# Kernel optimization log

Measured on AMD Instinct MI355X. Metric: run time of the kernel, lower is better.

The kernel has to match this reference:

```python
import jax, jax.numpy as jnp
import numpy as np


def setup_inputs() -> dict:
    key = jax.random.key(0)
    ks = jax.random.split(key, 5)
    B, T, D = 2048, 128, 512
    x = jax.random.normal(ks[0], (B, T, D), dtype=jnp.float32)
    h0 = jnp.zeros((1, B, 1), dtype=jnp.float32)
    w_ih = jax.random.normal(ks[1], (3, D), dtype=jnp.float32) * (1.0 / np.sqrt(D))
    w_hh = jax.random.normal(ks[2], (3, 1), dtype=jnp.float32)
    b_ih = jax.random.normal(ks[3], (3,), dtype=jnp.float32) * 0.1
    b_hh = jax.random.normal(ks[4], (3,), dtype=jnp.float32) * 0.1
    return {"x": x, "h0": h0, "w_ih": w_ih, "w_hh": w_hh, "b_ih": b_ih, "b_hh": b_hh}


def reference(x, h0, w_ih, w_hh, b_ih, b_hh):
    # PyTorch GRU, hidden_size=1, num_layers=1, batch_first=True.
    # Precompute the input projection for all timesteps: [B, T, 3] (gates r, z, n).
    gi = jnp.einsum('btd,gd->btg', x, w_ih) + b_ih

    def step(h, gi_t):
        # h: [B, 1]; gi_t: [B, 3]
        gh = h @ w_hh.T + b_hh                      # [B, 3]
        r = jax.nn.sigmoid(gi_t[:, 0:1] + gh[:, 0:1])
        z = jax.nn.sigmoid(gi_t[:, 1:2] + gh[:, 1:2])
        n = jnp.tanh(gi_t[:, 2:3] + r * gh[:, 2:3])
        h_new = (1.0 - z) * n + z * h               # [B, 1]
        return h_new, h_new

    _, outs = jax.lax.scan(step, h0[0], jnp.swapaxes(gi, 0, 1))  # [T, B, 1]
    out = jnp.swapaxes(outs, 0, 1)                                # [B, T, 1]
    # out.mean(0) -> [T, 1]; split into T scalars ('t0'..'tT-1') == squeezed vector [T]
    return out.mean(axis=0).squeeze(-1)
```

## Files before the change

kernel.cpp:

```cpp
#include <hip/hip_runtime.h>
#include <math.h>

#define BB 2048
#define TT 128
#define DD 512
#define NTASK (BB * TT)

__global__ __launch_bounds__(256) void gi_kernel(const float* __restrict__ x,
                                                 const float* __restrict__ w_ih,
                                                 float* __restrict__ gr,
                                                 float* __restrict__ gz,
                                                 float* __restrict__ gn) {
    const int lane   = threadIdx.x & 63;
    const int wave   = blockIdx.x * (blockDim.x >> 6) + (threadIdx.x >> 6);
    const int nwaves = (gridDim.x * blockDim.x) >> 6;

    const int doff = lane * 8;
    const float4 wr0 = *(const float4*)(w_ih + 0 * DD + doff);
    const float4 wr1 = *(const float4*)(w_ih + 0 * DD + doff + 4);
    const float4 wz0 = *(const float4*)(w_ih + 1 * DD + doff);
    const float4 wz1 = *(const float4*)(w_ih + 1 * DD + doff + 4);
    const float4 wn0 = *(const float4*)(w_ih + 2 * DD + doff);
    const float4 wn1 = *(const float4*)(w_ih + 2 * DD + doff + 4);

    for (int task = wave; task < NTASK; task += nwaves) {
        const float* xp = x + (size_t)task * DD + doff;
        const float4 x0 = *(const float4*)(xp);
        const float4 x1 = *(const float4*)(xp + 4);

        float sr = x0.x * wr0.x + x0.y * wr0.y + x0.z * wr0.z + x0.w * wr0.w +
                   x1.x * wr1.x + x1.y * wr1.y + x1.z * wr1.z + x1.w * wr1.w;
        float sz = x0.x * wz0.x + x0.y * wz0.y + x0.z * wz0.z + x0.w * wz0.w +
                   x1.x * wz1.x + x1.y * wz1.y + x1.z * wz1.z + x1.w * wz1.w;
        float sn = x0.x * wn0.x + x0.y * wn0.y + x0.z * wn0.z + x0.w * wn0.w +
                   x1.x * wn1.x + x1.y * wn1.y + x1.z * wn1.z + x1.w * wn1.w;

        #pragma unroll
        for (int off = 32; off > 0; off >>= 1) {
            sr += __shfl_xor(sr, off);
            sz += __shfl_xor(sz, off);
            sn += __shfl_xor(sn, off);
        }

        if (lane == 0) {
            const int b = task >> 7;
            const int t = task & (TT - 1);
            gr[t * BB + b] = sr;
            gz[t * BB + b] = sz;
            gn[t * BB + b] = sn;
        }
    }
}

__global__ __launch_bounds__(64) void gru_kernel(const float* __restrict__ gr,
                                                 const float* __restrict__ gz,
                                                 const float* __restrict__ gn,
                                                 const float* __restrict__ h0,
                                                 const float* __restrict__ w_hh,
                                                 const float* __restrict__ b_ih,
                                                 const float* __restrict__ b_hh,
                                                 float* __restrict__ out) {
    const int b = blockIdx.x * 64 + threadIdx.x;

    const float whr = w_hh[0], whz = w_hh[1], whn = w_hh[2];
    const float br  = b_ih[0] + b_hh[0];
    const float bz  = b_ih[1] + b_hh[1];
    const float bin_= b_ih[2];
    const float bhn = b_hh[2];

    float h = h0[b];

    for (int t = 0; t < TT; ++t) {
        const float ir  = gr[t * BB + b] + br  + h * whr;
        const float iz  = gz[t * BB + b] + bz  + h * whz;
        const float ghn = h * whn + bhn;

        const float r = 1.0f / (1.0f + expf(-ir));
        const float z = 1.0f / (1.0f + expf(-iz));
        const float n = tanhf(gn[t * BB + b] + b_ih[2] - bin_ + bin_ + r * ghn);

        h = (1.0f - z) * n + z * h;

        float s = h;
        #pragma unroll
        for (int off = 32; off > 0; off >>= 1) s += __shfl_xor(s, off);
        if (threadIdx.x == 0) atomicAdd(out + t, s * (1.0f / (float)BB));
    }
}

extern "C" void kernel_launch(void* const* d_in, const int* in_sizes, int n_in,
                              void* d_out, int out_size, void* d_ws, size_t ws_size,
                              hipStream_t stream) {
    const float* x    = (const float*)d_in[0];
    const float* h0   = (const float*)d_in[1];
    const float* w_ih = (const float*)d_in[2];
    const float* w_hh = (const float*)d_in[3];
    const float* b_ih = (const float*)d_in[4];
    const float* b_hh = (const float*)d_in[5];
    float* out = (float*)d_out;

    float* gr = (float*)d_ws;
    float* gz = gr + NTASK;
    float* gn = gz + NTASK;

    hipMemsetAsync(d_out, 0, (size_t)out_size * sizeof(float), stream);

    gi_kernel<<<2048, 256, 0, stream>>>(x, w_ih, gr, gz, gn);
    gru_kernel<<<BB / 64, 64, 0, stream>>>(gr, gz, gn, h0, w_hh, b_ih, b_hh, out);
}
```

Measured before the change: 804.6 us.

## Process two rows per wave in projection, fold output zeroing, block-reduce in GRU

The input-projection kernel now handles two (b,t) rows per wave iteration, putting more loads in flight to better saturate memory bandwidth on the large x read. The memset launch is removed and the output is zeroed inside the first kernel. The recurrent kernel uses 256-thread blocks with a shared-memory reduction, which cuts the number of atomics per timestep but adds two barriers per step and leaves only 8 blocks in flight.

```diff
diff --git a/kernel.cpp b/kernel.cpp
--- a/kernel.cpp
+++ b/kernel.cpp
@@ -10,7 +10,10 @@
                                                  const float* __restrict__ w_ih,
                                                  float* __restrict__ gr,
                                                  float* __restrict__ gz,
-                                                 float* __restrict__ gn) {
+                                                 float* __restrict__ gn,
+                                                 float* __restrict__ out) {
+    if (blockIdx.x == 0 && threadIdx.x < TT) out[threadIdx.x] = 0.0f;
+
     const int lane   = threadIdx.x & 63;
     const int wave   = blockIdx.x * (blockDim.x >> 6) + (threadIdx.x >> 6);
     const int nwaves = (gridDim.x * blockDim.x) >> 6;
@@ -23,10 +26,14 @@
     const float4 wn0 = *(const float4*)(w_ih + 2 * DD + doff);
     const float4 wn1 = *(const float4*)(w_ih + 2 * DD + doff + 4);
 
-    for (int task = wave; task < NTASK; task += nwaves) {
-        const float* xp = x + (size_t)task * DD + doff;
+    for (int task = wave; task < NTASK; task += 2 * nwaves) {
+        const int task2 = task + nwaves;
+        const float* xp  = x + (size_t)task  * DD + doff;
+        const float* xq  = x + (size_t)task2 * DD + doff;
         const float4 x0 = *(const float4*)(xp);
         const float4 x1 = *(const float4*)(xp + 4);
+        const float4 y0 = *(const float4*)(xq);
+        const float4 y1 = *(const float4*)(xq + 4);
 
         float sr = x0.x * wr0.x + x0.y * wr0.y + x0.z * wr0.z + x0.w * wr0.w +
                    x1.x * wr1.x + x1.y * wr1.y + x1.z * wr1.z + x1.w * wr1.w;
@@ -34,57 +41,86 @@
                    x1.x * wz1.x + x1.y * wz1.y + x1.z * wz1.z + x1.w * wz1.w;
         float sn = x0.x * wn0.x + x0.y * wn0.y + x0.z * wn0.z + x0.w * wn0.w +
                    x1.x * wn1.x + x1.y * wn1.y + x1.z * wn1.z + x1.w * wn1.w;
+        float tr = y0.x * wr0.x + y0.y * wr0.y + y0.z * wr0.z + y0.w * wr0.w +
+                   y1.x * wr1.x + y1.y * wr1.y + y1.z * wr1.z + y1.w * wr1.w;
+        float tz = y0.x * wz0.x + y0.y * wz0.y + y0.z * wz0.z + y0.w * wz0.w +
+                   y1.x * wz1.x + y1.y * wz1.y + y1.z * wz1.z + y1.w * wz1.w;
+        float tn = y0.x * wn0.x + y0.y * wn0.y + y0.z * wn0.z + y0.w * wn0.w +
+                   y1.x * wn1.x + y1.y * wn1.y + y1.z * wn1.z + y1.w * wn1.w;
 
         #pragma unroll
         for (int off = 32; off > 0; off >>= 1) {
             sr += __shfl_xor(sr, off);
             sz += __shfl_xor(sz, off);
             sn += __shfl_xor(sn, off);
+            tr += __shfl_xor(tr, off);
+            tz += __shfl_xor(tz, off);
+            tn += __shfl_xor(tn, off);
         }
 
         if (lane == 0) {
-            const int b = task >> 7;
-            const int t = task & (TT - 1);
-            gr[t * BB + b] = sr;
-            gz[t * BB + b] = sz;
-            gn[t * BB + b] = sn;
+            {
+                const int b = task >> 7, t = task & (TT - 1);
+                gr[t * BB + b] = sr;
+                gz[t * BB + b] = sz;
+                gn[t * BB + b] = sn;
+            }
+            {
+                const int b = task2 >> 7, t = task2 & (TT - 1);
+                gr[t * BB + b] = tr;
+                gz[t * BB + b] = tz;
+                gn[t * BB + b] = tn;
+            }
         }
     }
 }
 
-__global__ __launch_bounds__(64) void gru_kernel(const float* __restrict__ gr,
-                                                 const float* __restrict__ gz,
-                                                 const float* __restrict__ gn,
-                                                 const float* __restrict__ h0,
-                                                 const float* __restrict__ w_hh,
-                                                 const float* __restrict__ b_ih,
-                                                 const float* __restrict__ b_hh,
-                                                 float* __restrict__ out) {
-    const int b = blockIdx.x * 64 + threadIdx.x;
+__global__ __launch_bounds__(256) void gru_kernel(const float* __restrict__ gr,
+                                                  const float* __restrict__ gz,
+                                                  const float* __restrict__ gn,
+                                                  const float* __restrict__ h0,
+                                                  const float* __restrict__ w_hh,
+                                                  const float* __restrict__ b_ih,
+                                                  const float* __restrict__ b_hh,
+                                                  float* __restrict__ out) {
+    const int b    = blockIdx.x * 256 + threadIdx.x;
+    const int lane = threadIdx.x & 63;
+    const int wid  = threadIdx.x >> 6;
+    __shared__ float red[4];
 
     const float whr = w_hh[0], whz = w_hh[1], whn = w_hh[2];
     const float br  = b_ih[0] + b_hh[0];
     const float bz  = b_ih[1] + b_hh[1];
-    const float bin_= b_ih[2];
+    const float bn  = b_ih[2];
     const float bhn = b_hh[2];
 
     float h = h0[b];
 
     for (int t = 0; t < TT; ++t) {
-        const float ir  = gr[t * BB + b] + br  + h * whr;
-        const float iz  = gz[t * BB + b] + bz  + h * whz;
+        const float gir = gr[t * BB + b];
+        const float giz = gz[t * BB + b];
+        const float gin = gn[t * BB + b];
+
+        const float ir  = gir + br + h * whr;
+        const float iz  = giz + bz + h * whz;
         const float ghn = h * whn + bhn;
 
         const float r = 1.0f / (1.0f + expf(-ir));
         const float z = 1.0f / (1.0f + expf(-iz));
-        const float n = tanhf(gn[t * BB + b] + b_ih[2] - bin_ + bin_ + r * ghn);
+        const float n = tanhf(gin + bn + r * ghn);
 
         h = (1.0f - z) * n + z * h;
 
         float s = h;
         #pragma unroll
         for (int off = 32; off > 0; off >>= 1) s += __shfl_xor(s, off);
-        if (threadIdx.x == 0) atomicAdd(out + t, s * (1.0f / (float)BB));
+        if (lane == 0) red[wid] = s;
+        __syncthreads();
+        if (threadIdx.x == 0) {
+            const float blk = red[0] + red[1] + red[2] + red[3];
+            atomicAdd(out + t, blk * (1.0f / (float)BB));
+        }
+        __syncthreads();
     }
 }
 
@@ -103,8 +139,6 @@
     float* gz = gr + NTASK;
     float* gn = gz + NTASK;
 
-    hipMemsetAsync(d_out, 0, (size_t)out_size * sizeof(float), stream);
-
-    gi_kernel<<<2048, 256, 0, stream>>>(x, w_ih, gr, gz, gn);
-    gru_kernel<<<BB / 64, 64, 0, stream>>>(gr, gz, gn, h0, w_hh, b_ih, b_hh, out);
+    gi_kernel<<<2048, 256, 0, stream>>>(x, w_ih, gr, gz, gn, out);
+    gru_kernel<<<BB / 256, 256, 0, stream>>>(gr, gz, gn, h0, w_hh, b_ih, b_hh, out);
 }
```

Result: no change. 816.8 us (+1.5%).

## Fuse input projection and GRU recurrence into one kernel per batch group

Applied to the files above, without the earlier changes.

Merges the projection and recurrence kernels into one. Each block handles 4 batch rows: one wave per row computes the gate projections for all timesteps into shared memory, two timesteps per iteration. Four threads then run the serial recurrence from shared memory, and the per-timestep sums are reduced into the output with one atomic per timestep per block. This removes the global round trip of the gate workspace and one launch, but the serial recurrence now runs on only 4 threads per block while the rest of the block waits.

```diff
diff --git a/kernel.cpp b/kernel.cpp
--- a/kernel.cpp
+++ b/kernel.cpp
@@ -4,16 +4,21 @@
 #define BB 2048
 #define TT 128
 #define DD 512
-#define NTASK (BB * TT)
+#define BPB 4
 
-__global__ __launch_bounds__(256) void gi_kernel(const float* __restrict__ x,
+__global__ __launch_bounds__(256) void gru_fused(const float* __restrict__ x,
                                                  const float* __restrict__ w_ih,
-                                                 float* __restrict__ gr,
-                                                 float* __restrict__ gz,
-                                                 float* __restrict__ gn) {
-    const int lane   = threadIdx.x & 63;
-    const int wave   = blockIdx.x * (blockDim.x >> 6) + (threadIdx.x >> 6);
-    const int nwaves = (gridDim.x * blockDim.x) >> 6;
+                                                 const float* __restrict__ h0,
+                                                 const float* __restrict__ w_hh,
+                                                 const float* __restrict__ b_ih,
+                                                 const float* __restrict__ b_hh,
+                                                 float* __restrict__ out) {
+    __shared__ float gi_s[BPB * (TT * 3 + 1)];
+    __shared__ float hall[TT * BPB];
+
+    const int lane = threadIdx.x & 63;
+    const int wid  = threadIdx.x >> 6;
+    const int b    = blockIdx.x * BPB + wid;
 
     const int doff = lane * 8;
     const float4 wr0 = *(const float4*)(w_ih + 0 * DD + doff);
@@ -23,10 +28,14 @@
     const float4 wn0 = *(const float4*)(w_ih + 2 * DD + doff);
     const float4 wn1 = *(const float4*)(w_ih + 2 * DD + doff + 4);
 
-    for (int task = wave; task < NTASK; task += nwaves) {
-        const float* xp = x + (size_t)task * DD + doff;
+    float* gw = gi_s + wid * (TT * 3 + 1);
+
+    for (int t = 0; t < TT; t += 2) {
+        const float* xp = x + ((size_t)b * TT + t) * DD + doff;
         const float4 x0 = *(const float4*)(xp);
         const float4 x1 = *(const float4*)(xp + 4);
+        const float4 y0 = *(const float4*)(xp + DD);
+        const float4 y1 = *(const float4*)(xp + DD + 4);
 
         float sr = x0.x * wr0.x + x0.y * wr0.y + x0.z * wr0.z + x0.w * wr0.w +
                    x1.x * wr1.x + x1.y * wr1.y + x1.z * wr1.z + x1.w * wr1.w;
@@ -34,57 +43,61 @@
                    x1.x * wz1.x + x1.y * wz1.y + x1.z * wz1.z + x1.w * wz1.w;
         float sn = x0.x * wn0.x + x0.y * wn0.y + x0.z * wn0.z + x0.w * wn0.w +
                    x1.x * wn1.x + x1.y * wn1.y + x1.z * wn1.z + x1.w * wn1.w;
+        float tr = y0.x * wr0.x + y0.y * wr0.y + y0.z * wr0.z + y0.w * wr0.w +
+                   y1.x * wr1.x + y1.y * wr1.y + y1.z * wr1.z + y1.w * wr1.w;
+        float tz = y0.x * wz0.x + y0.y * wz0.y + y0.z * wz0.z + y0.w * wz0.w +
+                   y1.x * wz1.x + y1.y * wz1.y + y1.z * wz1.z + y1.w * wz1.w;
+        float tn = y0.x * wn0.x + y0.y * wn0.y + y0.z * wn0.z + y0.w * wn0.w +
+                   y1.x * wn1.x + y1.y * wn1.y + y1.z * wn1.z + y1.w * wn1.w;
 
         #pragma unroll
         for (int off = 32; off > 0; off >>= 1) {
             sr += __shfl_xor(sr, off);
             sz += __shfl_xor(sz, off);
             sn += __shfl_xor(sn, off);
+            tr += __shfl_xor(tr, off);
+            tz += __shfl_xor(tz, off);
+            tn += __shfl_xor(tn, off);
         }
 
         if (lane == 0) {
-            const int b = task >> 7;
-            const int t = task & (TT - 1);
-            gr[t * BB + b] = sr;
-            gz[t * BB + b] = sz;
-            gn[t * BB + b] = sn;
+            gw[(t    ) * 3 + 0] = sr;
+            gw[(t    ) * 3 + 1] = sz;
+            gw[(t    ) * 3 + 2] = sn;
+            gw[(t + 1) * 3 + 0] = tr;
+            gw[(t + 1) * 3 + 1] = tz;
+            gw[(t + 1) * 3 + 2] = tn;
         }
     }
-}
+    __syncthreads();
 
-__global__ __launch_bounds__(64) void gru_kernel(const float* __restrict__ gr,
-                                                 const float* __restrict__ gz,
-                                                 const float* __restrict__ gn,
-                                                 const float* __restrict__ h0,
-                                                 const float* __restrict__ w_hh,
-                                                 const float* __restrict__ b_ih,
-                                                 const float* __restrict__ b_hh,
-                                                 float* __restrict__ out) {
-    const int b = blockIdx.x * 64 + threadIdx.x;
+    if (threadIdx.x < BPB) {
+        const int bl = threadIdx.x;
+        const float whr = w_hh[0], whz = w_hh[1], whn = w_hh[2];
+        const float br  = b_ih[0] + b_hh[0];
+        const float bz  = b_ih[1] + b_hh[1];
+        const float bn  = b_ih[2];
+        const float bhn = b_hh[2];
+        const float* g  = gi_s + bl * (TT * 3 + 1);
 
-    const float whr = w_hh[0], whz = w_hh[1], whn = w_hh[2];
-    const float br  = b_ih[0] + b_hh[0];
-    const float bz  = b_ih[1] + b_hh[1];
-    const float bin_= b_ih[2];
-    const float bhn = b_hh[2];
+        float h = h0[blockIdx.x * BPB + bl];
+        for (int t = 0; t < TT; ++t) {
+            const float ir  = g[t * 3 + 0] + br + h * whr;
+            const float iz  = g[t * 3 + 1] + bz + h * whz;
+            const float ghn = h * whn + bhn;
+            const float r = 1.0f / (1.0f + expf(-ir));
+            const float z = 1.0f / (1.0f + expf(-iz));
+            const float n = tanhf(g[t * 3 + 2] + bn + r * ghn);
+            h = (1.0f - z) * n + z * h;
+            hall[t * BPB + bl] = h;
+        }
+    }
+    __syncthreads();
 
-    float h = h0[b];
-
-    for (int t = 0; t < TT; ++t) {
-        const float ir  = gr[t * BB + b] + br  + h * whr;
-        const float iz  = gz[t * BB + b] + bz  + h * whz;
-        const float ghn = h * whn + bhn;
-
-        const float r = 1.0f / (1.0f + expf(-ir));
-        const float z = 1.0f / (1.0f + expf(-iz));
-        const float n = tanhf(gn[t * BB + b] + b_ih[2] - bin_ + bin_ + r * ghn);
-
-        h = (1.0f - z) * n + z * h;
-
-        float s = h;
-        #pragma unroll
-        for (int off = 32; off > 0; off >>= 1) s += __shfl_xor(s, off);
-        if (threadIdx.x == 0) atomicAdd(out + t, s * (1.0f / (float)BB));
+    if (threadIdx.x < TT) {
+        const float4 hv = *(const float4*)(hall + threadIdx.x * BPB);
+        const float s = hv.x + hv.y + hv.z + hv.w;
+        atomicAdd(out + threadIdx.x, s * (1.0f / (float)BB));
     }
 }
 
@@ -99,12 +112,7 @@
     const float* b_hh = (const float*)d_in[5];
     float* out = (float*)d_out;
 
-    float* gr = (float*)d_ws;
-    float* gz = gr + NTASK;
-    float* gn = gz + NTASK;
-
     hipMemsetAsync(d_out, 0, (size_t)out_size * sizeof(float), stream);
 
-    gi_kernel<<<2048, 256, 0, stream>>>(x, w_ih, gr, gz, gn);
-    gru_kernel<<<BB / 64, 64, 0, stream>>>(gr, gz, gn, h0, w_hh, b_ih, b_hh, out);
+    gru_fused<<<BB / BPB, 256, 0, stream>>>(x, w_ih, h0, w_hh, b_ih, b_hh, out);
 }
```

Result: faster. 745.6 us (-7.3%).
